# Performance work log

Measured on AMD Instinct MI355X. Metric: run time of the kernel, lower is better.

## Reference

```python
import jax, jax.numpy as jnp
import numpy as np

B, C, H, W = 2, 1024, 64, 64
E, TOP_K = 8, 2
FFN = C  # ffn_dim = in_channels; hidden_dim = out_channels = in_channels


def setup_inputs() -> dict:
    key = jax.random.key(0)
    ks = jax.random.split(key, 5)
    s = 0.02
    return {
        "hidden_states": jax.random.normal(ks[0], (B, C, H, W), jnp.float32),
        "gate_w": jax.random.normal(ks[1], (E, C), jnp.float32) * s,   # torch Linear weight [out,in]
        "w1": jax.random.normal(ks[2], (E, FFN, C), jnp.float32) * s,
        "w2": jax.random.normal(ks[3], (E, C, FFN), jnp.float32) * s,
        "w3": jax.random.normal(ks[4], (E, FFN, C), jnp.float32) * s,
    }


def reference(hidden_states, gate_w, w1, w2, w3):
    b, c = hidden_states.shape[0], hidden_states.shape[1]
    space = hidden_states.shape[2:]
    # (B, C, H, W) -> (B, H, W, C) -> (T, C)
    x = jnp.transpose(hidden_states, (0, 2, 3, 1)).reshape(-1, c)

    # Router: softmax in float32, top-k, renormalize (matches torch)
    logits = x @ gate_w.T                                   # [T, E]
    probs = jax.nn.softmax(logits.astype(jnp.float32), axis=-1)
    rw, sel = jax.lax.top_k(probs, TOP_K)                   # [T, K]
    rw = rw / jnp.sum(rw, axis=-1, keepdims=True)
    rw = rw.astype(x.dtype)

    # Combine weights per expert: zero where expert not selected -> exact
    # equivalence with gather/scatter dispatch (full capacity, no drops).
    combine = jnp.sum(jax.nn.one_hot(sel, E, dtype=x.dtype) * rw[..., None], axis=1)  # [T, E]

    out = jnp.zeros_like(x)
    for e in range(E):  # small fixed expert loop
        h = jax.nn.gelu(x @ w1[e].T, approximate=False) * (x @ w3[e].T)  # SwiGLU-style [T, FFN]
        out = out + combine[:, e:e + 1] * (h @ w2[e].T)

    out = out.reshape(b, *space, c)
    return jnp.transpose(out, (0, 3, 1, 2))  # (B, C, H, W)
```

## Files before the change

### kernel.cpp

```cpp
#include <hip/hip_runtime.h>
#include <hip/hip_bf16.h>
#include <math.h>

#define BB 2
#define CC 1024
#define HH 64
#define WW 64
#define HWH (HH*WW)
#define TT (BB*HWH)
#define EE 8
#define FFN 1024
#define MAXTILES 71
#define HCAP (MAXTILES*256)

typedef __bf16 bf16x8 __attribute__((ext_vector_type(8)));
typedef float  f32x4  __attribute__((ext_vector_type(4)));

__device__ __forceinline__ void gl_lds16(const __bf16* g, __bf16* l) {
    __builtin_amdgcn_global_load_lds(
        (const __attribute__((address_space(1))) void*)g,
        (__attribute__((address_space(3))) void*)l, 16, 0, 0);
}

__device__ __forceinline__ void barrier_raw() {
    asm volatile("" ::: "memory");
    __builtin_amdgcn_s_barrier();
    asm volatile("" ::: "memory");
}

__device__ __forceinline__ int xcd_swz(int orig, int nwg) {
    const int q = nwg >> 3, r = nwg & 7, x = orig & 7, o8 = orig >> 3;
    return (x < r ? x * (q + 1) : r * (q + 1) + (x - r) * q) + o8;
}

__device__ __forceinline__ float gelu_fast(float a) {
    const float a2 = a * a;
    const float t  = a * fmaf(0.044715f, a2, 1.0f);
    const float u  = __builtin_amdgcn_exp2f(t * -2.30220795f);
    return a * __builtin_amdgcn_rcpf(1.0f + u);
}

#define WAITV(N) asm volatile("s_waitcnt vmcnt(" #N ")" ::: "memory")
#define PRIO1()  __builtin_amdgcn_s_setprio(1)
#define PRIO0()  __builtin_amdgcn_s_setprio(0)

#define CVB 12288
#define XPB 8192
#define RTB 512
__global__ __launch_bounds__(256) void k_prep(
    const float* __restrict__ hs, const float* __restrict__ gate_w,
    const float* __restrict__ w1, const float* __restrict__ w2,
    const float* __restrict__ w3,
    __bf16* __restrict__ w1b, __bf16* __restrict__ w2b,
    __bf16* __restrict__ w3b, __bf16* __restrict__ X,
    float* __restrict__ logP) {
    __shared__ float sm[2112];
    const int bid = blockIdx.x;
    const int tid = threadIdx.x;

    if (bid < CVB) {
        const float* s; __bf16* d; int lb = bid;
        if (lb < 4096)      { s = w1; d = w1b; }
        else if (lb < 8192) { s = w2; d = w2b; lb -= 4096; }
        else                { s = w3; d = w3b; lb -= 8192; }
        const size_t i = (size_t)lb * 2048 + (size_t)tid * 8;
        const f32x4 v0 = *(const f32x4*)&s[i];
        const f32x4 v1 = *(const f32x4*)&s[i + 4];
        bf16x8 o;
#pragma unroll
        for (int j = 0; j < 4; ++j) { o[j] = (__bf16)v0[j]; o[4 + j] = (__bf16)v1[j]; }
        *(bf16x8*)&d[i] = o;
    } else if (bid < CVB + XPB) {
        const int lb  = bid - CVB;
        const int hw0 = (lb & 127) * 32;
        const int c0  = ((lb >> 7) & 31) * 32;
        const int b   = lb >> 12;
        float (*tile)[33] = (float(*)[33])sm;
        const int tx = tid & 31, ty = tid >> 5;
        const float* src = hs + ((size_t)b * CC + c0) * HWH + hw0;
#pragma unroll
        for (int i = 0; i < 4; ++i)
            tile[ty + i * 8][tx] = src[(size_t)(ty + i * 8) * HWH + tx];
        __syncthreads();
        __bf16* dst = X + ((size_t)b * HWH + hw0) * CC + c0;
#pragma unroll
        for (int i = 0; i < 4; ++i) {
            const int hwl = ty + i * 8;
            dst[(size_t)hwl * CC + tx] = (__bf16)tile[tx][hwl];
        }
    } else {
        const int lb  = bid - (CVB + XPB);
        const int q   = lb & 3;
        const int t64 = lb >> 2;
        float* g = sm;
        for (int i = tid; i < 2048; i += 256)
            g[i] = gate_w[(size_t)(i >> 8) * CC + q * 256 + (i & 255)];
        __syncthreads();
        const int q2 = tid >> 6, tl = tid & 63;
        const int t  = t64 * 64 + tl;
        const int b  = t >> 12, hw = t & 4095;
        const float* xp = hs + (size_t)b * CC * HWH + hw;
        float l[EE];
#pragma unroll
        for (int e = 0; e < EE; ++e) l[e] = 0.0f;
        const int cbase = q * 256 + q2 * 64;
        for (int c2 = 0; c2 < 64; ++c2) {
            const float xv = xp[(size_t)(cbase + c2) * HWH];
#pragma unroll
            for (int e = 0; e < EE; ++e) l[e] += xv * g[e * 256 + q2 * 64 + c2];
        }
        float* dst = logP + ((size_t)(q * 4 + q2) * TT + t) * 8;
        f32x4 a, c;
#pragma unroll
        for (int e = 0; e < 4; ++e) { a[e] = l[e]; c[e] = l[4 + e]; }
        *(f32x4*)dst = a;
        *(f32x4*)&dst[4] = c;
    }
}

__global__ __launch_bounds__(256) void k_top2(const float* __restrict__ logP,
                                              int* __restrict__ cnt,
                                              int* __restrict__ idxl,
                                              int* __restrict__ tokE,
                                              int* __restrict__ tokP,
                                              float* __restrict__ tokW) {
    __shared__ int lcnt[EE], lbase[EE];
    const int tid = threadIdx.x;
    const int t   = blockIdx.x * 256 + tid;
    if (tid < EE) lcnt[tid] = 0;
    __syncthreads();

    float l[EE];
#pragma unroll
    for (int e = 0; e < EE; ++e) l[e] = 0.0f;
#pragma unroll
    for (int pq = 0; pq < 16; ++pq) {
        const float* src = logP + ((size_t)pq * TT + t) * 8;
        const f32x4 a = *(const f32x4*)src;
        const f32x4 c = *(const f32x4*)&src[4];
#pragma unroll
        for (int e = 0; e < 4; ++e) { l[e] += a[e]; l[4 + e] += c[e]; }
    }

    int e1 = 0; float v1 = l[0];
#pragma unroll
    for (int e = 1; e < EE; ++e) { if (l[e] > v1) { v1 = l[e]; e1 = e; } }
    int e2 = -1; float v2 = -1e30f;
#pragma unroll
    for (int e = 0; e < EE; ++e) { if (e != e1 && l[e] > v2) { v2 = l[e]; e2 = e; } }

    const float p2 = __expf(v2 - v1);
    const float rs = 1.0f / (1.0f + p2);

    const int m1 = atomicAdd(&lcnt[e1], 1);
    const int m2 = atomicAdd(&lcnt[e2], 1);
    __syncthreads();
    if (tid < EE) lbase[tid] = atomicAdd(&cnt[tid], lcnt[tid]);
    __syncthreads();
    const int p1pos = lbase[e1] + m1;
    const int p2pos = lbase[e2] + m2;

    idxl[e1 * TT + p1pos] = t;
    idxl[e2 * TT + p2pos] = t;
    tokE[t] = e1 | (e2 << 8);
    tokP[2 * t]     = p1pos;
    tokP[2 * t + 1] = p2pos;
    tokW[2 * t]     = rs;
    tokW[2 * t + 1] = p2 * rs;
}

#define GT_TILE(SR, SS, KB, STG, WC) do {                                     \
    if (STG) {                                                                \
        gl_lds16(gA0 + (KB), &sA[SS][stA]);                                   \
        gl_lds16(gA1 + (KB), &sA[SS][stA + 4096]);                            \
        gl_lds16(gB0 + (KB), &sB[SS][stA]);                                   \
    }                                                                         \
    bf16x8 af[4], bv[4];                                                      \
    _Pragma("unroll") for (int f_ = 0; f_ < 4; ++f_) {                        \
        af[f_] = *(const bf16x8*)&sA[SR][aoff + f_ * 512];                    \
        bv[f_] = *(const bf16x8*)&sB[SR][boff + f_ * 512];                    \
    }                                                                         \
    PRIO1();                                                                  \
    _Pragma("unroll") for (int m_ = 0; m_ < 4; ++m_)                          \
    _Pragma("unroll") for (int n_ = 0; n_ < 4; ++n_)                          \
        acc[m_][n_] = __builtin_amdgcn_mfma_f32_16x16x32_bf16(                \
            af[m_], bv[n_], acc[m_][n_], 0, 0, 0);                            \
    PRIO0();                                                                  \
    WC;                                                                       \
    barrier_raw();                                                            \
} while (0)

__global__ __launch_bounds__(512, 4)
void k_gemm1(const __bf16* __restrict__ X, const __bf16* __restrict__ w1b,
             const __bf16* __restrict__ w3b, const int* __restrict__ cnt,
             const int* __restrict__ idxl, __bf16* __restrict__ H) {
    const int lid = blockIdx.y * 16 + blockIdx.x;
    const int wg  = xcd_swz(lid, 16 * MAXTILES);
    const int n0  = (wg & 15) * 64;
    int ty = wg >> 4;
    int e = -1, mt = 0, goff = 0, acc_rows = 0;
#pragma unroll
    for (int ee = 0; ee < EE; ++ee) {
        const int me = (cnt[ee] + 255) >> 8;
        if (ty >= 0 && ty < me) { e = ee; mt = ty << 8; goff = acc_rows; }
        ty -= me;
        acc_rows += me << 8;
    }
    if (e < 0) return;
    const int cntE = cnt[e];
    const __bf16* W1 = w1b + (size_t)e * FFN * CC;
    const __bf16* W3 = w3b + (size_t)e * FFN * CC;

    __shared__ __align__(16) __bf16 sA[3][8192];
    __shared__ __align__(16) __bf16 sB[3][4096];

    const int tid  = threadIdx.x;
    const int lane = tid & 63, wave = tid >> 6;
    const int l15  = lane & 15, lq = lane >> 4;
    const int wm   = wave & 3;
    const int wq   = wave >> 2;
    const int rsw  = (lq ^ ((l15 >> 1) & 3)) * 8;

    const int csw  = ((tid & 3) ^ ((tid >> 3) & 3)) * 8;
    const int cswb = ((lane & 3) ^ ((lane >> 3) & 3)) * 8;

    int pr0 = mt + (tid >> 2);        if (pr0 > cntE - 1) pr0 = cntE - 1;
    int pr1 = mt + 128 + (tid >> 2);  if (pr1 > cntE - 1) pr1 = cntE - 1;
    const __bf16* gA0 = X + (size_t)idxl[e * TT + pr0] * CC + csw;
    const __bf16* gA1 = X + (size_t)idxl[e * TT + pr1] * CC + csw;
    const __bf16* WB  = (wave & 1) ? W3 : W1;
    const __bf16* gB0 = WB + (size_t)(n0 + (wave >> 1) * 16 + (lane >> 2)) * CC + cswb;

    const int stA  = wave * 512;
    const int aoff = (wm * 64 + l15) * 32 + rsw;
    const int boff = (wq * 64 + l15) * 32 + rsw;

    f32x4 acc[4][4] = {};

    gl_lds16(gA0,      &sA[0][stA]); gl_lds16(gA1,      &sA[0][stA + 4096]);
    gl_lds16(gB0,      &sB[0][stA]);
    gl_lds16(gA0 + 32, &sA[1][stA]); gl_lds16(gA1 + 32, &sA[1][stA + 4096]);
    gl_lds16(gB0 + 32, &sB[1][stA]);
    WAITV(3);
    barrier_raw();

    int kb = 64;
    for (int it = 0; it < 10; ++it) {
        GT_TILE(0, 2, kb, 1, WAITV(3)); kb += 32;
        GT_TILE(1, 0, kb, 1, WAITV(3)); kb += 32;
        GT_TILE(2, 1, kb, 1, WAITV(3)); kb += 32;
    }
    GT_TILE(0, 0, 0, 0, WAITV(0));
    GT_TILE(1, 0, 0, 0, (void)0);

#pragma unroll
    for (int mf = 0; mf < 4; ++mf) {
        const int gr  = goff + mt + wm * 64 + mf * 16 + lq * 4;
        const int col = n0 + wq * 32 + l15;
#pragma unroll
        for (int r = 0; r < 4; ++r) {
            const float a0 = acc[mf][0][r], c0 = acc[mf][1][r];
            const float a1 = acc[mf][2][r], c1 = acc[mf][3][r];
            H[(size_t)(gr + r) * FFN + col]      = (__bf16)(gelu_fast(a0) * c0);
            H[(size_t)(gr + r) * FFN + col + 16] = (__bf16)(gelu_fast(a1) * c1);
        }
    }
}

__global__ __launch_bounds__(512, 4)
void k_gemm2(const __bf16* __restrict__ H, const __bf16* __restrict__ w2b,
             const int* __restrict__ cnt, __bf16* __restrict__ Z) {
    const int lid = blockIdx.y * 8 + blockIdx.x;
    const int wg  = xcd_swz(lid, 8 * MAXTILES);
    const int n0  = (wg & 7) * 128;
    int ty = wg >> 3;
    int e = -1, mt = 0, goff = 0, acc_rows = 0;
#pragma unroll
    for (int ee = 0; ee < EE; ++ee) {
        const int me = (cnt[ee] + 255) >> 8;
        if (ty >= 0 && ty < me) { e = ee; mt = ty << 8; goff = acc_rows; }
        ty -= me;
        acc_rows += me << 8;
    }
    if (e < 0) return;
    const __bf16* W2 = w2b + (size_t)e * CC * FFN;
    const __bf16* Ar = H + (size_t)(goff + mt) * FFN;

    __shared__ __align__(16) __bf16 sA[3][8192];
    __shared__ __align__(16) __bf16 sB[3][4096];

    const int tid  = threadIdx.x;
    const int lane = tid & 63, wave = tid >> 6;
    const int l15  = lane & 15, lq = lane >> 4;
    const int wm   = wave & 3;
    const int wq   = wave >> 2;
    const int rsw  = (lq ^ ((l15 >> 1) & 3)) * 8;
    const int csw  = ((tid & 3) ^ ((tid >> 3) & 3)) * 8;
    const int cswb = ((lane & 3) ^ ((lane >> 3) & 3)) * 8;

    const __bf16* gA0 = Ar + (size_t)(tid >> 2) * FFN + csw;
    const __bf16* gA1 = Ar + (size_t)(128 + (tid >> 2)) * FFN + csw;
    const __bf16* gB0 = W2 + (size_t)(n0 + wave * 16 + (lane >> 2)) * FFN + cswb;

    const int stA  = wave * 512;
    const int aoff = (wm * 64 + l15) * 32 + rsw;
    const int boff = (wq * 64 + l15) * 32 + rsw;

    f32x4 acc[4][4] = {};

    gl_lds16(gA0,      &sA[0][stA]); gl_lds16(gA1,      &sA[0][stA + 4096]);
    gl_lds16(gB0,      &sB[0][stA]);
    gl_lds16(gA0 + 32, &sA[1][stA]); gl_lds16(gA1 + 32, &sA[1][stA + 4096]);
    gl_lds16(gB0 + 32, &sB[1][stA]);
    WAITV(3);
    barrier_raw();

    int kb = 64;
    for (int it = 0; it < 10; ++it) {
        GT_TILE(0, 2, kb, 1, WAITV(3)); kb += 32;
        GT_TILE(1, 0, kb, 1, WAITV(3)); kb += 32;
        GT_TILE(2, 1, kb, 1, WAITV(3)); kb += 32;
    }
    GT_TILE(0, 0, 0, 0, WAITV(0));
    GT_TILE(1, 0, 0, 0, (void)0);

#pragma unroll
    for (int mf = 0; mf < 4; ++mf) {
        const int gr = goff + mt + wm * 64 + mf * 16 + lq * 4;
#pragma unroll
        for (int nf = 0; nf < 4; ++nf) {
            const int col = n0 + wq * 64 + nf * 16 + l15;
#pragma unroll
            for (int r = 0; r < 4; ++r)
                Z[(size_t)(gr + r) * CC + col] = (__bf16)acc[mf][nf][r];
        }
    }
}

__global__ __launch_bounds__(256) void k_combine(const __bf16* __restrict__ Z,
                                                 const int* __restrict__ cnt,
                                                 const int* __restrict__ tokE,
                                                 const int* __restrict__ tokP,
                                                 const float* __restrict__ tokW,
                                                 float* __restrict__ out) {
    __shared__ float tile[32][33];
    __shared__ int s_pre[EE];
    const int tid = threadIdx.x;
    if (tid < EE) {
        int a = 0;
        for (int ee = 0; ee < tid; ++ee) a += ((cnt[ee] + 255) >> 8) << 8;
        s_pre[tid] = a;
    }
    __syncthreads();

    const int t0 = blockIdx.x * 32;
    const int c0 = blockIdx.y * 32;
    const int tx = tid & 31;
    const int ty = tid >> 5;

#pragma unroll
    for (int i = 0; i < 4; ++i) {
        const int tl = ty + 8 * i;
        const int t  = t0 + tl;
        const int ee = tokE[t];
        const int e1 = ee & 0xff, e2 = ee >> 8;
        const int r1 = s_pre[e1] + tokP[2 * t];
        const int r2 = s_pre[e2] + tokP[2 * t + 1];
        const float v = tokW[2 * t]     * (float)Z[(size_t)r1 * CC + c0 + tx]
                      + tokW[2 * t + 1] * (float)Z[(size_t)r2 * CC + c0 + tx];
        tile[tl][tx] = v;
    }
    __syncthreads();

    const int b   = t0 >> 12;
    const int hw0 = t0 & 4095;
#pragma unroll
    for (int i = 0; i < 4; ++i) {
        const int cl = ty + 8 * i;
        out[(size_t)b * CC * HWH + (size_t)(c0 + cl) * HWH + hw0 + tx] = tile[tx][cl];
    }
}

extern "C" void kernel_launch(void* const* d_in, const int* in_sizes, int n_in,
                              void* d_out, int out_size, void* d_ws, size_t ws_size,
                              hipStream_t stream) {
    const float* hs     = (const float*)d_in[0];
    const float* gate_w = (const float*)d_in[1];
    const float* w1     = (const float*)d_in[2];
    const float* w2     = (const float*)d_in[3];
    const float* w3     = (const float*)d_in[4];
    float* out = (float*)d_out;

    const size_t WSZ = (size_t)EE * FFN * CC * 2;
    char* ws = (char*)d_ws;
    __bf16* w2b  = (__bf16*)ws;
    __bf16* w1b  = (__bf16*)(ws + WSZ);
    __bf16* w3b  = (__bf16*)(ws + 2 * WSZ);
    __bf16* X    = (__bf16*)(ws + 3 * WSZ);
    __bf16* Zbuf = (__bf16*)(ws + WSZ);
    __bf16* Hbuf = (__bf16*)(ws + 4 * WSZ);
    float*  logP = (float*)Hbuf;
    char* p = ws + 4 * WSZ + (size_t)HCAP * FFN * 2;
    int*   idxl  = (int*)p;           p += (size_t)EE * TT * 4;
    int*   tokE  = (int*)p;           p += (size_t)TT * 4;
    int*   tokP  = (int*)p;           p += (size_t)2 * TT * 4;
    float* tokW  = (float*)p;         p += (size_t)2 * TT * 4;
    int*   cnt   = (int*)p;           p += 256;

    hipMemsetAsync(cnt, 0, EE * sizeof(int), stream);

    k_prep<<<CVB + XPB + RTB, 256, 0, stream>>>(
        hs, gate_w, w1, w2, w3, w1b, w2b, w3b, X, logP);
    k_top2<<<TT / 256, 256, 0, stream>>>(logP, cnt, idxl, tokE, tokP, tokW);

    k_gemm1<<<dim3(FFN / 64, MAXTILES), 512, 0, stream>>>(
        X, w1b, w3b, cnt, idxl, Hbuf);
    k_gemm2<<<dim3(CC / 128, MAXTILES), 512, 0, stream>>>(
        Hbuf, w2b, cnt, Zbuf);
    k_combine<<<dim3(TT / 32, CC / 32), 256, 0, stream>>>(
        Zbuf, cnt, tokE, tokP, tokW, out);
}
```

Before: 327.0 us.

## Fuse MoE GEMM1 and GEMM2 into a persistent kernel with per-tile flags

Adds a persistent kernel with 512 workgroups. Each workgroup first processes GEMM1 tiles (gate/up projections with GELU product), then GEMM2 tiles in reverse order. GEMM2 tiles wait on per-row-tile atomic completion counters instead of a kernel boundary. This removes one launch and the tail of the first GEMM, letting down-projection work overlap with the remaining up-projection work. It costs spin-wait latency, an extra Z buffer in the workspace, and a fallback path when the workspace is too small.

```diff
diff --git a/kernel.cpp b/kernel.cpp
--- a/kernel.cpp
+++ b/kernel.cpp
@@ -190,6 +190,32 @@
     barrier_raw();                                                            \
 } while (0)
 
+#define GT_KLOOP() do {                                                       \
+    gl_lds16(gA0,      &sA[0][stA]); gl_lds16(gA1,      &sA[0][stA + 4096]); \
+    gl_lds16(gB0,      &sB[0][stA]);                                          \
+    gl_lds16(gA0 + 32, &sA[1][stA]); gl_lds16(gA1 + 32, &sA[1][stA + 4096]); \
+    gl_lds16(gB0 + 32, &sB[1][stA]);                                          \
+    WAITV(3);                                                                 \
+    barrier_raw();                                                            \
+    int kb = 64;                                                              \
+    for (int t3 = 0; t3 < 10; ++t3) {                                         \
+        GT_TILE(0, 2, kb, 1, WAITV(3)); kb += 32;                             \
+        GT_TILE(1, 0, kb, 1, WAITV(3)); kb += 32;                             \
+        GT_TILE(2, 1, kb, 1, WAITV(3)); kb += 32;                             \
+    }                                                                         \
+    GT_TILE(0, 0, 0, 0, WAITV(0));                                            \
+    GT_TILE(1, 0, 0, 0, (void)0);                                             \
+} while (0)
+
+#define TILE_MAP(TIX, E, MT, GOFF) do {                                       \
+    int ty_ = (TIX); int ar_ = 0; E = 0; MT = 0; GOFF = 0;                    \
+    _Pragma("unroll") for (int ee_ = 0; ee_ < EE; ++ee_) {                    \
+        const int me_ = (cnt[ee_] + 255) >> 8;                                \
+        if (ty_ >= 0 && ty_ < me_) { E = ee_; MT = ty_ << 8; GOFF = ar_; }    \
+        ty_ -= me_; ar_ += me_ << 8;                                          \
+    }                                                                         \
+} while (0)
+
 __global__ __launch_bounds__(512, 4)
 void k_gemm1(const __bf16* __restrict__ X, const __bf16* __restrict__ w1b,
              const __bf16* __restrict__ w3b, const int* __restrict__ cnt,
@@ -197,94 +223,17 @@
     const int lid = blockIdx.y * 16 + blockIdx.x;
     const int wg  = xcd_swz(lid, 16 * MAXTILES);
     const int n0  = (wg & 15) * 64;
-    int ty = wg >> 4;
-    int e = -1, mt = 0, goff = 0, acc_rows = 0;
-#pragma unroll
-    for (int ee = 0; ee < EE; ++ee) {
-        const int me = (cnt[ee] + 255) >> 8;
-        if (ty >= 0 && ty < me) { e = ee; mt = ty << 8; goff = acc_rows; }
-        ty -= me;
-        acc_rows += me << 8;
-    }
-    if (e < 0) return;
+    int e, mt, goff;
+    TILE_MAP(wg >> 4, e, mt, goff);
+    {
+        int nT = 0;
+#pragma unroll
+        for (int ee = 0; ee < EE; ++ee) nT += (cnt[ee] + 255) >> 8;
+        if ((wg >> 4) >= nT) return;
+    }
     const int cntE = cnt[e];
     const __bf16* W1 = w1b + (size_t)e * FFN * CC;
     const __bf16* W3 = w3b + (size_t)e * FFN * CC;
-
-    __shared__ __align__(16) __bf16 sA[3][8192];
-    __shared__ __align__(16) __bf16 sB[3][4096];
-
-    const int tid  = threadIdx.x;
-    const int lane = tid & 63, wave = tid >> 6;
-    const int l15  = lane & 15, lq = lane >> 4;
-    const int wm   = wave & 3;
-    const int wq   = wave >> 2;
-    const int rsw  = (lq ^ ((l15 >> 1) & 3)) * 8;
-
-    const int csw  = ((tid & 3) ^ ((tid >> 3) & 3)) * 8;
-    const int cswb = ((lane & 3) ^ ((lane >> 3) & 3)) * 8;
-
-    int pr0 = mt + (tid >> 2);        if (pr0 > cntE - 1) pr0 = cntE - 1;
-    int pr1 = mt + 128 + (tid >> 2);  if (pr1 > cntE - 1) pr1 = cntE - 1;
-    const __bf16* gA0 = X + (size_t)idxl[e * TT + pr0] * CC + csw;
-    const __bf16* gA1 = X + (size_t)idxl[e * TT + pr1] * CC + csw;
-    const __bf16* WB  = (wave & 1) ? W3 : W1;
-    const __bf16* gB0 = WB + (size_t)(n0 + (wave >> 1) * 16 + (lane >> 2)) * CC + cswb;
-
-    const int stA  = wave * 512;
-    const int aoff = (wm * 64 + l15) * 32 + rsw;
-    const int boff = (wq * 64 + l15) * 32 + rsw;
-
-    f32x4 acc[4][4] = {};
-
-    gl_lds16(gA0,      &sA[0][stA]); gl_lds16(gA1,      &sA[0][stA + 4096]);
-    gl_lds16(gB0,      &sB[0][stA]);
-    gl_lds16(gA0 + 32, &sA[1][stA]); gl_lds16(gA1 + 32, &sA[1][stA + 4096]);
-    gl_lds16(gB0 + 32, &sB[1][stA]);
-    WAITV(3);
-    barrier_raw();
-
-    int kb = 64;
-    for (int it = 0; it < 10; ++it) {
-        GT_TILE(0, 2, kb, 1, WAITV(3)); kb += 32;
-        GT_TILE(1, 0, kb, 1, WAITV(3)); kb += 32;
-        GT_TILE(2, 1, kb, 1, WAITV(3)); kb += 32;
-    }
-    GT_TILE(0, 0, 0, 0, WAITV(0));
-    GT_TILE(1, 0, 0, 0, (void)0);
-
-#pragma unroll
-    for (int mf = 0; mf < 4; ++mf) {
-        const int gr  = goff + mt + wm * 64 + mf * 16 + lq * 4;
-        const int col = n0 + wq * 32 + l15;
-#pragma unroll
-        for (int r = 0; r < 4; ++r) {
-            const float a0 = acc[mf][0][r], c0 = acc[mf][1][r];
-            const float a1 = acc[mf][2][r], c1 = acc[mf][3][r];
-            H[(size_t)(gr + r) * FFN + col]      = (__bf16)(gelu_fast(a0) * c0);
-            H[(size_t)(gr + r) * FFN + col + 16] = (__bf16)(gelu_fast(a1) * c1);
-        }
-    }
-}
-
-__global__ __launch_bounds__(512, 4)
-void k_gemm2(const __bf16* __restrict__ H, const __bf16* __restrict__ w2b,
-             const int* __restrict__ cnt, __bf16* __restrict__ Z) {
-    const int lid = blockIdx.y * 8 + blockIdx.x;
-    const int wg  = xcd_swz(lid, 8 * MAXTILES);
-    const int n0  = (wg & 7) * 128;
-    int ty = wg >> 3;
-    int e = -1, mt = 0, goff = 0, acc_rows = 0;
-#pragma unroll
-    for (int ee = 0; ee < EE; ++ee) {
-        const int me = (cnt[ee] + 255) >> 8;
-        if (ty >= 0 && ty < me) { e = ee; mt = ty << 8; goff = acc_rows; }
-        ty -= me;
-        acc_rows += me << 8;
-    }
-    if (e < 0) return;
-    const __bf16* W2 = w2b + (size_t)e * CC * FFN;
-    const __bf16* Ar = H + (size_t)(goff + mt) * FFN;
 
     __shared__ __align__(16) __bf16 sA[3][8192];
     __shared__ __align__(16) __bf16 sB[3][4096];
@@ -298,6 +247,63 @@
     const int csw  = ((tid & 3) ^ ((tid >> 3) & 3)) * 8;
     const int cswb = ((lane & 3) ^ ((lane >> 3) & 3)) * 8;
 
+    int pr0 = mt + (tid >> 2);        if (pr0 > cntE - 1) pr0 = cntE - 1;
+    int pr1 = mt + 128 + (tid >> 2);  if (pr1 > cntE - 1) pr1 = cntE - 1;
+    const __bf16* gA0 = X + (size_t)idxl[e * TT + pr0] * CC + csw;
+    const __bf16* gA1 = X + (size_t)idxl[e * TT + pr1] * CC + csw;
+    const __bf16* WB  = (wave & 1) ? W3 : W1;
+    const __bf16* gB0 = WB + (size_t)(n0 + (wave >> 1) * 16 + (lane >> 2)) * CC + cswb;
+
+    const int stA  = wave * 512;
+    const int aoff = (wm * 64 + l15) * 32 + rsw;
+    const int boff = (wq * 64 + l15) * 32 + rsw;
+
+    f32x4 acc[4][4] = {};
+    GT_KLOOP();
+
+#pragma unroll
+    for (int mf = 0; mf < 4; ++mf) {
+        const int gr  = goff + mt + wm * 64 + mf * 16 + lq * 4;
+        const int col = n0 + wq * 32 + l15;
+#pragma unroll
+        for (int r = 0; r < 4; ++r) {
+            const float a0 = acc[mf][0][r], c0 = acc[mf][1][r];
+            const float a1 = acc[mf][2][r], c1 = acc[mf][3][r];
+            H[(size_t)(gr + r) * FFN + col]      = (__bf16)(gelu_fast(a0) * c0);
+            H[(size_t)(gr + r) * FFN + col + 16] = (__bf16)(gelu_fast(a1) * c1);
+        }
+    }
+}
+
+__global__ __launch_bounds__(512, 4)
+void k_gemm2(const __bf16* __restrict__ H, const __bf16* __restrict__ w2b,
+             const int* __restrict__ cnt, __bf16* __restrict__ Z) {
+    const int lid = blockIdx.y * 8 + blockIdx.x;
+    const int wg  = xcd_swz(lid, 8 * MAXTILES);
+    const int n0  = (wg & 7) * 128;
+    int e, mt, goff;
+    TILE_MAP(wg >> 3, e, mt, goff);
+    {
+        int nT = 0;
+#pragma unroll
+        for (int ee = 0; ee < EE; ++ee) nT += (cnt[ee] + 255) >> 8;
+        if ((wg >> 3) >= nT) return;
+    }
+    const __bf16* W2 = w2b + (size_t)e * CC * FFN;
+    const __bf16* Ar = H + (size_t)(goff + mt) * FFN;
+
+    __shared__ __align__(16) __bf16 sA[3][8192];
+    __shared__ __align__(16) __bf16 sB[3][4096];
+
+    const int tid  = threadIdx.x;
+    const int lane = tid & 63, wave = tid >> 6;
+    const int l15  = lane & 15, lq = lane >> 4;
+    const int wm   = wave & 3;
+    const int wq   = wave >> 2;
+    const int rsw  = (lq ^ ((l15 >> 1) & 3)) * 8;
+    const int csw  = ((tid & 3) ^ ((tid >> 3) & 3)) * 8;
+    const int cswb = ((lane & 3) ^ ((lane >> 3) & 3)) * 8;
+
     const __bf16* gA0 = Ar + (size_t)(tid >> 2) * FFN + csw;
     const __bf16* gA1 = Ar + (size_t)(128 + (tid >> 2)) * FFN + csw;
     const __bf16* gB0 = W2 + (size_t)(n0 + wave * 16 + (lane >> 2)) * FFN + cswb;
@@ -307,22 +313,7 @@
     const int boff = (wq * 64 + l15) * 32 + rsw;
 
     f32x4 acc[4][4] = {};
-
-    gl_lds16(gA0,      &sA[0][stA]); gl_lds16(gA1,      &sA[0][stA + 4096]);
-    gl_lds16(gB0,      &sB[0][stA]);
-    gl_lds16(gA0 + 32, &sA[1][stA]); gl_lds16(gA1 + 32, &sA[1][stA + 4096]);
-    gl_lds16(gB0 + 32, &sB[1][stA]);
-    WAITV(3);
-    barrier_raw();
-
-    int kb = 64;
-    for (int it = 0; it < 10; ++it) {
-        GT_TILE(0, 2, kb, 1, WAITV(3)); kb += 32;
-        GT_TILE(1, 0, kb, 1, WAITV(3)); kb += 32;
-        GT_TILE(2, 1, kb, 1, WAITV(3)); kb += 32;
-    }
-    GT_TILE(0, 0, 0, 0, WAITV(0));
-    GT_TILE(1, 0, 0, 0, (void)0);
+    GT_KLOOP();
 
 #pragma unroll
     for (int mf = 0; mf < 4; ++mf) {
@@ -334,6 +325,112 @@
             for (int r = 0; r < 4; ++r)
                 Z[(size_t)(gr + r) * CC + col] = (__bf16)acc[mf][nf][r];
         }
+    }
+}
+
+__global__ __launch_bounds__(512, 4)
+void k_moe(const __bf16* __restrict__ X, const __bf16* __restrict__ w1b,
+           const __bf16* __restrict__ w3b, const __bf16* __restrict__ w2b,
+           const int* __restrict__ cnt, const int* __restrict__ idxl,
+           __bf16* __restrict__ H, __bf16* __restrict__ Z,
+           int* __restrict__ done1) {
+    __shared__ __align__(16) __bf16 sA[3][8192];
+    __shared__ __align__(16) __bf16 sB[3][4096];
+
+    const int tid  = threadIdx.x;
+    const int lane = tid & 63, wave = tid >> 6;
+    const int l15  = lane & 15, lq = lane >> 4;
+    const int wm   = wave & 3;
+    const int wq   = wave >> 2;
+    const int rsw  = (lq ^ ((l15 >> 1) & 3)) * 8;
+    const int csw  = ((tid & 3) ^ ((tid >> 3) & 3)) * 8;
+    const int cswb = ((lane & 3) ^ ((lane >> 3) & 3)) * 8;
+    const int stA  = wave * 512;
+    const int aoff = (wm * 64 + l15) * 32 + rsw;
+    const int boff = (wq * 64 + l15) * 32 + rsw;
+
+    int nT = 0;
+#pragma unroll
+    for (int ee = 0; ee < EE; ++ee) nT += (cnt[ee] + 255) >> 8;
+    const int n1 = nT * 16, n2 = nT * 8;
+    const int base = xcd_swz(blockIdx.x, 512);
+
+    for (int it = base; it < n1; it += 512) {
+        const int tix = it >> 4;
+        const int n0  = (it & 15) * 64;
+        int e, mt, goff;
+        TILE_MAP(tix, e, mt, goff);
+        const int cntE = cnt[e];
+        const __bf16* W1 = w1b + (size_t)e * FFN * CC;
+        const __bf16* W3 = w3b + (size_t)e * FFN * CC;
+
+        int pr0 = mt + (tid >> 2);        if (pr0 > cntE - 1) pr0 = cntE - 1;
+        int pr1 = mt + 128 + (tid >> 2);  if (pr1 > cntE - 1) pr1 = cntE - 1;
+        const __bf16* gA0 = X + (size_t)idxl[e * TT + pr0] * CC + csw;
+        const __bf16* gA1 = X + (size_t)idxl[e * TT + pr1] * CC + csw;
+        const __bf16* WB  = (wave & 1) ? W3 : W1;
+        const __bf16* gB0 = WB + (size_t)(n0 + (wave >> 1) * 16 + (lane >> 2)) * CC + cswb;
+
+        f32x4 acc[4][4] = {};
+        GT_KLOOP();
+
+#pragma unroll
+        for (int mf = 0; mf < 4; ++mf) {
+            const int gr  = goff + mt + wm * 64 + mf * 16 + lq * 4;
+            const int col = n0 + wq * 32 + l15;
+#pragma unroll
+            for (int r = 0; r < 4; ++r) {
+                const float a0 = acc[mf][0][r], c0 = acc[mf][1][r];
+                const float a1 = acc[mf][2][r], c1 = acc[mf][3][r];
+                H[(size_t)(gr + r) * FFN + col]      = (__bf16)(gelu_fast(a0) * c0);
+                H[(size_t)(gr + r) * FFN + col + 16] = (__bf16)(gelu_fast(a1) * c1);
+            }
+        }
+        __threadfence();
+        __syncthreads();
+        if (tid == 0)
+            __hip_atomic_fetch_add(&done1[tix], 1, __ATOMIC_RELEASE,
+                                   __HIP_MEMORY_SCOPE_AGENT);
+    }
+
+    for (int it = 511 - base; it < n2; it += 512) {
+        const int tix = it >> 3;
+        const int n0  = (it & 7) * 128;
+        if (tid == 0) {
+            int guard = 0;
+            while (__hip_atomic_load(&done1[tix], __ATOMIC_RELAXED,
+                                     __HIP_MEMORY_SCOPE_AGENT) < 16 &&
+                   ++guard < (1 << 24))
+                __builtin_amdgcn_s_sleep(8);
+            (void)__hip_atomic_load(&done1[tix], __ATOMIC_ACQUIRE,
+                                    __HIP_MEMORY_SCOPE_AGENT);
+        }
+        __syncthreads();
+
+        int e, mt, goff;
+        TILE_MAP(tix, e, mt, goff);
+        const __bf16* W2 = w2b + (size_t)e * CC * FFN;
+        const __bf16* Ar = H + (size_t)(goff + mt) * FFN;
+
+        const __bf16* gA0 = Ar + (size_t)(tid >> 2) * FFN + csw;
+        const __bf16* gA1 = Ar + (size_t)(128 + (tid >> 2)) * FFN + csw;
+        const __bf16* gB0 = W2 + (size_t)(n0 + wave * 16 + (lane >> 2)) * FFN + cswb;
+
+        f32x4 acc[4][4] = {};
+        GT_KLOOP();
+
+#pragma unroll
+        for (int mf = 0; mf < 4; ++mf) {
+            const int gr = goff + mt + wm * 64 + mf * 16 + lq * 4;
+#pragma unroll
+            for (int nf = 0; nf < 4; ++nf) {
+                const int col = n0 + wq * 64 + nf * 16 + l15;
+#pragma unroll
+                for (int r = 0; r < 4; ++r)
+                    Z[(size_t)(gr + r) * CC + col] = (__bf16)acc[mf][nf][r];
+            }
+        }
+        __syncthreads();
     }
 }
 
@@ -392,31 +489,45 @@
     float* out = (float*)d_out;
 
     const size_t WSZ = (size_t)EE * FFN * CC * 2;
+    const size_t HFB = (size_t)HCAP * FFN * 2;
     char* ws = (char*)d_ws;
     __bf16* w2b  = (__bf16*)ws;
     __bf16* w1b  = (__bf16*)(ws + WSZ);
     __bf16* w3b  = (__bf16*)(ws + 2 * WSZ);
     __bf16* X    = (__bf16*)(ws + 3 * WSZ);
-    __bf16* Zbuf = (__bf16*)(ws + WSZ);
     __bf16* Hbuf = (__bf16*)(ws + 4 * WSZ);
     float*  logP = (float*)Hbuf;
-    char* p = ws + 4 * WSZ + (size_t)HCAP * FFN * 2;
+    char* p = ws + 4 * WSZ + HFB;
     int*   idxl  = (int*)p;           p += (size_t)EE * TT * 4;
     int*   tokE  = (int*)p;           p += (size_t)TT * 4;
     int*   tokP  = (int*)p;           p += (size_t)2 * TT * 4;
     float* tokW  = (float*)p;         p += (size_t)2 * TT * 4;
-    int*   cnt   = (int*)p;           p += 256;
-
-    hipMemsetAsync(cnt, 0, EE * sizeof(int), stream);
+    int*   cnt   = (int*)p;           p += 1024;
+    int*   done1 = (int*)p;           p += 2048;
+    const size_t off_end = (size_t)(p - ws);
+    const size_t need_fused = off_end + (size_t)HCAP * CC * 2;
+
+    const bool fused = (ws_size >= need_fused);
+    __bf16* Zf   = (__bf16*)(ws + off_end);
+    __bf16* Zovl = (__bf16*)(ws + WSZ);
+
+    hipMemsetAsync(cnt, 0, 1024 + 2048, stream);
 
     k_prep<<<CVB + XPB + RTB, 256, 0, stream>>>(
         hs, gate_w, w1, w2, w3, w1b, w2b, w3b, X, logP);
     k_top2<<<TT / 256, 256, 0, stream>>>(logP, cnt, idxl, tokE, tokP, tokW);
 
-    k_gemm1<<<dim3(FFN / 64, MAXTILES), 512, 0, stream>>>(
-        X, w1b, w3b, cnt, idxl, Hbuf);
-    k_gemm2<<<dim3(CC / 128, MAXTILES), 512, 0, stream>>>(
-        Hbuf, w2b, cnt, Zbuf);
-    k_combine<<<dim3(TT / 32, CC / 32), 256, 0, stream>>>(
-        Zbuf, cnt, tokE, tokP, tokW, out);
-}
+    if (fused) {
+        k_moe<<<512, 512, 0, stream>>>(X, w1b, w3b, w2b, cnt, idxl,
+                                       Hbuf, Zf, done1);
+        k_combine<<<dim3(TT / 32, CC / 32), 256, 0, stream>>>(
+            Zf, cnt, tokE, tokP, tokW, out);
+    } else {
+        k_gemm1<<<dim3(FFN / 64, MAXTILES), 512, 0, stream>>>(
+            X, w1b, w3b, cnt, idxl, Hbuf);
+        k_gemm2<<<dim3(CC / 128, MAXTILES), 512, 0, stream>>>(
+            Hbuf, w2b, cnt, Zovl);
+        k_combine<<<dim3(TT / 32, CC / 32), 256, 0, stream>>>(
+            Zovl, cnt, tokE, tokP, tokW, out);
+    }
+}
```

Result: slower. 809.3 us (+147.5%).
